# Kernel tuning notes

Measured on AMD Instinct MI355X. Metric: run time of the kernel, lower is better.

Reference implementation:

```python
import jax, jax.numpy as jnp
import numpy as np

IN_FEATURES = 512
OUT_FEATURES = 10
NEURONS_STRUCTURES = [64, 128, 256, 512]
REPETITIONS = 5
NUM_ACTIVATIONS = 4  # relu, tanh, sigmoid, gelu (exact erf, matching torch nn.GELU)
NUM_MODELS = NUM_ACTIVATIONS * REPETITIONS * len(NEURONS_STRUCTURES)  # 80
TOTAL_HIDDEN = sum(NEURONS_STRUCTURES) * REPETITIONS * NUM_ACTIVATIONS  # 19200
BATCH = 1024


def _build_neuron_model_id():
    # Mirrors ParallelMLPs.__init__ construction order:
    # for act -> for rep -> for structure: assign consecutive model ids
    ids = []
    m = 0
    for _act in range(NUM_ACTIVATIONS):
        for _rep in range(REPETITIONS):
            for n in NEURONS_STRUCTURES:
                ids += [m] * n
                m += 1
    return np.asarray(ids, dtype=np.int32)


def setup_inputs() -> dict:
    key = jax.random.key(0)
    k1, k2, k3, k4, k5 = jax.random.split(key, 5)
    x = jax.random.normal(k1, (BATCH, IN_FEATURES), dtype=jnp.float32)
    hidden_w = jax.random.normal(k2, (TOTAL_HIDDEN, IN_FEATURES), dtype=jnp.float32) * 0.05
    hidden_b = jax.random.normal(k3, (TOTAL_HIDDEN,), dtype=jnp.float32) * 0.05
    out_w = jax.random.normal(k4, (OUT_FEATURES, TOTAL_HIDDEN), dtype=jnp.float32) * 0.05
    out_b = jax.random.normal(k5, (NUM_MODELS, OUT_FEATURES), dtype=jnp.float32) * 0.05
    neuron_model_id = jnp.asarray(_build_neuron_model_id())
    return {"x": x, "hidden_w": hidden_w, "hidden_b": hidden_b,
            "out_w": out_w, "out_b": out_b, "neuron_model_id": neuron_model_id}


def reference(x, hidden_w, hidden_b, out_w, out_b, neuron_model_id):
    # Shared hidden linear: [B, H]
    h = x @ hidden_w.T + hidden_b
    # Per-block activations on equal contiguous chunks of the hidden dim
    split = TOTAL_HIDDEN // NUM_ACTIVATIONS
    acts = [jax.nn.relu, jnp.tanh, jax.nn.sigmoid,
            lambda t: jax.nn.gelu(t, approximate=False)]
    a = jnp.concatenate(
        [f(h[:, i * split:(i + 1) * split]) for i, f in enumerate(acts)], axis=1)
    # Ragged grouped out-projection: contrib[h, b, o] = a[b, h] * out_w[o, h]
    contrib = a.T[:, :, None] * out_w.T[:, None, :]  # [H, B, O]
    grouped = jax.ops.segment_sum(contrib, neuron_model_id,
                                  num_segments=NUM_MODELS)  # [M, B, O]
    return jnp.transpose(grouped, (1, 0, 2)) + out_b[None, :, :]  # [B, M, O]
```

## Files before the change

### kernel.cpp

```cpp
#include <hip/hip_runtime.h>
#include <hip/hip_bf16.h>
#include <cstdint>
#include <cstddef>


typedef unsigned short u16;
typedef unsigned int u32;
typedef __bf16 bf16x8 __attribute__((ext_vector_type(8)));
typedef float f32x4 __attribute__((ext_vector_type(4)));

__device__ __forceinline__ u16 f2bf(float f) {
  u32 u = __builtin_bit_cast(u32, f);
  u += 0x7fffu + ((u >> 16) & 1u);
  return (u16)(u >> 16);
}

__device__ __forceinline__ void async16(void* l, const void* g) {
  __builtin_amdgcn_global_load_lds(
      (__attribute__((address_space(1))) void*)(void*)g,
      (__attribute__((address_space(3))) void*)l, 16, 0, 0);
}

__global__ __launch_bounds__(256) void cvt_kernel(
    const float4* __restrict__ xs, uint2* __restrict__ xd, int nx4,
    const float4* __restrict__ ws, uint2* __restrict__ wd, int nw4) {
  int i = blockIdx.x * blockDim.x + threadIdx.x;
  if (i >= nx4 + nw4) return;
  const float4* s; uint2* d; int j;
  if (i < nx4) { s = xs; d = xd; j = i; }
  else         { s = ws; d = wd; j = i - nx4; }
  float4 f = s[j];
  uint2 o;
  o.x = (u32)f2bf(f.x) | ((u32)f2bf(f.y) << 16);
  o.y = (u32)f2bf(f.z) | ((u32)f2bf(f.w) << 16);
  d[j] = o;
}

__global__ __launch_bounds__(256, 2) void gemm_act_kernel(
    const u16* __restrict__ A,
    const u16* __restrict__ Bw,
    const float* __restrict__ hbias,
    u16* __restrict__ aout) {
  __shared__ char lds[65536];
  const int t = threadIdx.x;
  const int lane = t & 63;
  const int w = t >> 6;
  const int c = blockIdx.x & 7;
  const int L = c * 150 + (blockIdx.x >> 3);
  const int bx = L >> 3;
  const int by = L & 7;
  const int row0 = by * 128;
  const int col0 = bx * 128;
  const int wr = w >> 1, wc = w & 1;

  f32x4 acc[4][4];
#pragma unroll
  for (int m = 0; m < 4; ++m)
#pragma unroll
    for (int n = 0; n < 4; ++n)
#pragma unroll
      for (int r = 0; r < 4; ++r) acc[m][n][r] = 0.f;

  const int srow = t >> 3;
  const int sc8 = t & 7;

  auto stage = [&](int buf, int kt) {
    const int c8 = sc8 ^ (srow & 7);
    const int k0 = kt * 64 + c8 * 8;
#pragma unroll
    for (int i = 0; i < 4; ++i) {
      int row = i * 32 + srow;
      async16(lds + buf * 16384 + i * 4096 + w * 1024,
              A + (size_t)(row0 + row) * 512 + k0);
      async16(lds + 32768 + buf * 16384 + i * 4096 + w * 1024,
              Bw + (size_t)(col0 + row) * 512 + k0);
    }
  };

  const int il = lane & 15, q = lane >> 4;

  auto compute = [&](int buf) {
    const char* bA = lds + buf * 16384;
    const char* bB = lds + 32768 + buf * 16384;
#pragma unroll
    for (int ks = 0; ks < 2; ++ks) {
      bf16x8 av[4], bv[4];
#pragma unroll
      for (int m = 0; m < 4; ++m) {
        int row = wr * 64 + m * 16 + il;
        av[m] = *(const bf16x8*)(bA + row * 128 +
                                 ((ks * 64 + q * 16) ^ ((row & 7) << 4)));
      }
#pragma unroll
      for (int n = 0; n < 4; ++n) {
        int row = wc * 64 + n * 16 + il;
        bv[n] = *(const bf16x8*)(bB + row * 128 +
                                 ((ks * 64 + q * 16) ^ ((row & 7) << 4)));
      }
#pragma unroll
      for (int m = 0; m < 4; ++m)
#pragma unroll
        for (int n = 0; n < 4; ++n)
          acc[m][n] = __builtin_amdgcn_mfma_f32_16x16x32_bf16(av[m], bv[n],
                                                              acc[m][n], 0, 0, 0);
    }
  };

  stage(0, 0);
  stage(1, 1);
#pragma unroll
  for (int kt = 0; kt < 8; ++kt) {
    if (kt < 7) asm volatile("s_waitcnt vmcnt(8)" ::: "memory");
    else        asm volatile("s_waitcnt vmcnt(0)" ::: "memory");
    __builtin_amdgcn_s_barrier();
    compute(kt & 1);
    asm volatile("" ::: "memory");
    __builtin_amdgcn_s_barrier();
    if (kt < 6) stage(kt & 1, kt + 2);
  }

#pragma unroll
  for (int n = 0; n < 4; ++n) {
    int gcol = col0 + wc * 64 + n * 16 + il;
    int act = gcol / 4800;
    float bias = hbias[gcol];
#pragma unroll
    for (int m = 0; m < 4; ++m) {
      int growb = row0 + wr * 64 + m * 16 + q * 4;
#pragma unroll
      for (int r = 0; r < 4; ++r) {
        float v = acc[m][n][r] + bias;
        float o;
        if (act == 0)      o = fmaxf(v, 0.f);
        else if (act == 1) {
          float e = __expf(-2.f * fabsf(v));
          o = copysignf((1.f - e) / (1.f + e), v);
        }
        else if (act == 2) o = 1.f / (1.f + __expf(-v));
        else               o = 0.5f * v * (1.f + erff(v * 0.70710678118f));
        aout[(size_t)(growb + r) * 19200 + gcol] = f2bf(o);
      }
    }
  }
}

__global__ __launch_bounds__(256) void layer2_kernel(
    const u16* __restrict__ a,
    const float* __restrict__ ow,
    const float* __restrict__ ob,
    float* __restrict__ out) {
  const int t = threadIdx.x;
  const int lane = t & 63;
  const int w = t >> 6;
  const int m = blockIdx.x % 80;
  const int bt = blockIdx.x / 80;
  const int b0 = bt * 64 + w * 16;
  const int s = m & 3;
  const int rep = (m >> 2) % 5;
  const int act = m / 20;
  const int seg0 = act * 4800 + rep * 960 + 64 * ((1 << s) - 1);
  const int K = 64 << s;
  const int il = lane & 15, q = lane >> 4;

  f32x4 acc = {0.f, 0.f, 0.f, 0.f};
  const u16* arow = a + (size_t)(b0 + il) * 19200 + seg0 + q * 8;
  const float* wrow = ow + il * 19200 + seg0 + q * 8;
  const bool wvalid = il < 10;

  for (int k0 = 0; k0 < K; k0 += 32) {
    bf16x8 af = *(const bf16x8*)(arow + k0);
    union { bf16x8 v; u16 u[8]; } bb;
    if (wvalid) {
      float4 f0 = *(const float4*)(wrow + k0);
      float4 f1 = *(const float4*)(wrow + k0 + 4);
      bb.u[0] = f2bf(f0.x); bb.u[1] = f2bf(f0.y);
      bb.u[2] = f2bf(f0.z); bb.u[3] = f2bf(f0.w);
      bb.u[4] = f2bf(f1.x); bb.u[5] = f2bf(f1.y);
      bb.u[6] = f2bf(f1.z); bb.u[7] = f2bf(f1.w);
    } else {
#pragma unroll
      for (int j = 0; j < 8; ++j) bb.u[j] = 0;
    }
    acc = __builtin_amdgcn_mfma_f32_16x16x32_bf16(af, bb.v, acc, 0, 0, 0);
  }

  if (il < 10) {
    float bias = ob[m * 10 + il];
#pragma unroll
    for (int r = 0; r < 4; ++r)
      out[(size_t)(b0 + q * 4 + r) * 800 + m * 10 + il] = acc[r] + bias;
  }
}

extern "C" void kernel_launch(void* const* d_in, const int* in_sizes, int n_in,
                              void* d_out, int out_size, void* d_ws, size_t ws_size,
                              hipStream_t stream) {
  const float* x = (const float*)d_in[0];
  const float* hw = (const float*)d_in[1];
  const float* hb = (const float*)d_in[2];
  const float* ow = (const float*)d_in[3];
  const float* ob = (const float*)d_in[4];
  float* out = (float*)d_out;

  char* ws = (char*)d_ws;
  u16* xb = (u16*)ws;
  u16* wb = (u16*)(ws + 1048576);
  u16* ab = (u16*)(ws + 1048576 + 19660800);

  const int nx4 = (1024 * 512) / 4;
  const int nw4 = (19200 * 512) / 4;
  const int tot = nx4 + nw4;
  cvt_kernel<<<tot / 256, 256, 0, stream>>>((const float4*)x, (uint2*)xb, nx4,
                                            (const float4*)hw, (uint2*)wb, nw4);
  gemm_act_kernel<<<1200, 256, 0, stream>>>(xb, wb, hb, ab);
  layer2_kernel<<<1280, 256, 0, stream>>>(ab, ow, ob, out);
}
```

Before: 177.0 us.

## Halve GEMM K-tile to raise occupancy and unroll layer2 with dual accumulators

The hidden GEMM now stages K=32 slices instead of K=64, which halves LDS to 32 KB. The launch-bounds occupancy target rises from 2 to 5 blocks per CU, and the swizzle, staging loads and wait counts are adjusted to match. The goal is more resident waves to hide global-load latency, at the cost of twice as many barriers and smaller loads per stage. The layer-2 kernel processes 64 K per iteration with two independent MFMA accumulators to increase ILP.

```diff
diff --git a/kernel.cpp b/kernel.cpp
--- a/kernel.cpp
+++ b/kernel.cpp
@@ -36,12 +36,12 @@
   d[j] = o;
 }
 
-__global__ __launch_bounds__(256, 2) void gemm_act_kernel(
+__global__ __launch_bounds__(256, 5) void gemm_act_kernel(
     const u16* __restrict__ A,
     const u16* __restrict__ Bw,
     const float* __restrict__ hbias,
     u16* __restrict__ aout) {
-  __shared__ char lds[65536];
+  __shared__ char lds[32768];
   const int t = threadIdx.x;
   const int lane = t & 63;
   const int w = t >> 6;
@@ -61,18 +61,18 @@
 #pragma unroll
       for (int r = 0; r < 4; ++r) acc[m][n][r] = 0.f;
 
-  const int srow = t >> 3;
-  const int sc8 = t & 7;
+  const int srow = t >> 2;
+  const int sc4 = t & 3;
 
   auto stage = [&](int buf, int kt) {
-    const int c8 = sc8 ^ (srow & 7);
-    const int k0 = kt * 64 + c8 * 8;
-#pragma unroll
-    for (int i = 0; i < 4; ++i) {
-      int row = i * 32 + srow;
-      async16(lds + buf * 16384 + i * 4096 + w * 1024,
+    const int c4 = sc4 ^ ((srow >> 1) & 3);
+    const int k0 = kt * 32 + c4 * 8;
+#pragma unroll
+    for (int i = 0; i < 2; ++i) {
+      int row = i * 64 + srow;
+      async16(lds + buf * 8192 + i * 4096 + w * 1024,
               A + (size_t)(row0 + row) * 512 + k0);
-      async16(lds + 32768 + buf * 16384 + i * 4096 + w * 1024,
+      async16(lds + 16384 + buf * 8192 + i * 4096 + w * 1024,
               Bw + (size_t)(col0 + row) * 512 + k0);
     }
   };
@@ -80,43 +80,40 @@
   const int il = lane & 15, q = lane >> 4;
 
   auto compute = [&](int buf) {
-    const char* bA = lds + buf * 16384;
-    const char* bB = lds + 32768 + buf * 16384;
-#pragma unroll
-    for (int ks = 0; ks < 2; ++ks) {
-      bf16x8 av[4], bv[4];
-#pragma unroll
-      for (int m = 0; m < 4; ++m) {
-        int row = wr * 64 + m * 16 + il;
-        av[m] = *(const bf16x8*)(bA + row * 128 +
-                                 ((ks * 64 + q * 16) ^ ((row & 7) << 4)));
-      }
-#pragma unroll
-      for (int n = 0; n < 4; ++n) {
-        int row = wc * 64 + n * 16 + il;
-        bv[n] = *(const bf16x8*)(bB + row * 128 +
-                                 ((ks * 64 + q * 16) ^ ((row & 7) << 4)));
-      }
-#pragma unroll
-      for (int m = 0; m < 4; ++m)
-#pragma unroll
-        for (int n = 0; n < 4; ++n)
-          acc[m][n] = __builtin_amdgcn_mfma_f32_16x16x32_bf16(av[m], bv[n],
-                                                              acc[m][n], 0, 0, 0);
-    }
+    const char* bA = lds + buf * 8192;
+    const char* bB = lds + 16384 + buf * 8192;
+    bf16x8 av[4], bv[4];
+#pragma unroll
+    for (int m = 0; m < 4; ++m) {
+      int row = wr * 64 + m * 16 + il;
+      av[m] = *(const bf16x8*)(bA + row * 64 +
+                               ((q * 16) ^ (((row >> 1) & 3) << 4)));
+    }
+#pragma unroll
+    for (int n = 0; n < 4; ++n) {
+      int row = wc * 64 + n * 16 + il;
+      bv[n] = *(const bf16x8*)(bB + row * 64 +
+                               ((q * 16) ^ (((row >> 1) & 3) << 4)));
+    }
+#pragma unroll
+    for (int m = 0; m < 4; ++m)
+#pragma unroll
+      for (int n = 0; n < 4; ++n)
+        acc[m][n] = __builtin_amdgcn_mfma_f32_16x16x32_bf16(av[m], bv[n],
+                                                            acc[m][n], 0, 0, 0);
   };
 
   stage(0, 0);
   stage(1, 1);
-#pragma unroll
-  for (int kt = 0; kt < 8; ++kt) {
-    if (kt < 7) asm volatile("s_waitcnt vmcnt(8)" ::: "memory");
-    else        asm volatile("s_waitcnt vmcnt(0)" ::: "memory");
+#pragma unroll 4
+  for (int kt = 0; kt < 16; ++kt) {
+    if (kt < 15) asm volatile("s_waitcnt vmcnt(4)" ::: "memory");
+    else         asm volatile("s_waitcnt vmcnt(0)" ::: "memory");
     __builtin_amdgcn_s_barrier();
     compute(kt & 1);
     asm volatile("" ::: "memory");
     __builtin_amdgcn_s_barrier();
-    if (kt < 6) stage(kt & 1, kt + 2);
+    if (kt < 14) stage(kt & 1, kt + 2);
   }
 
 #pragma unroll
@@ -162,33 +159,42 @@
   const int K = 64 << s;
   const int il = lane & 15, q = lane >> 4;
 
-  f32x4 acc = {0.f, 0.f, 0.f, 0.f};
+  f32x4 acc0 = {0.f, 0.f, 0.f, 0.f};
+  f32x4 acc1 = {0.f, 0.f, 0.f, 0.f};
   const u16* arow = a + (size_t)(b0 + il) * 19200 + seg0 + q * 8;
   const float* wrow = ow + il * 19200 + seg0 + q * 8;
   const bool wvalid = il < 10;
 
-  for (int k0 = 0; k0 < K; k0 += 32) {
-    bf16x8 af = *(const bf16x8*)(arow + k0);
-    union { bf16x8 v; u16 u[8]; } bb;
+  for (int k0 = 0; k0 < K; k0 += 64) {
+    bf16x8 af0 = *(const bf16x8*)(arow + k0);
+    bf16x8 af1 = *(const bf16x8*)(arow + k0 + 32);
+    union { bf16x8 v; u16 u[8]; } b0u, b1u;
     if (wvalid) {
       float4 f0 = *(const float4*)(wrow + k0);
       float4 f1 = *(const float4*)(wrow + k0 + 4);
-      bb.u[0] = f2bf(f0.x); bb.u[1] = f2bf(f0.y);
-      bb.u[2] = f2bf(f0.z); bb.u[3] = f2bf(f0.w);
-      bb.u[4] = f2bf(f1.x); bb.u[5] = f2bf(f1.y);
-      bb.u[6] = f2bf(f1.z); bb.u[7] = f2bf(f1.w);
+      float4 f2 = *(const float4*)(wrow + k0 + 32);
+      float4 f3 = *(const float4*)(wrow + k0 + 36);
+      b0u.u[0] = f2bf(f0.x); b0u.u[1] = f2bf(f0.y);
+      b0u.u[2] = f2bf(f0.z); b0u.u[3] = f2bf(f0.w);
+      b0u.u[4] = f2bf(f1.x); b0u.u[5] = f2bf(f1.y);
+      b0u.u[6] = f2bf(f1.z); b0u.u[7] = f2bf(f1.w);
+      b1u.u[0] = f2bf(f2.x); b1u.u[1] = f2bf(f2.y);
+      b1u.u[2] = f2bf(f2.z); b1u.u[3] = f2bf(f2.w);
+      b1u.u[4] = f2bf(f3.x); b1u.u[5] = f2bf(f3.y);
+      b1u.u[6] = f2bf(f3.z); b1u.u[7] = f2bf(f3.w);
     } else {
 #pragma unroll
-      for (int j = 0; j < 8; ++j) bb.u[j] = 0;
-    }
-    acc = __builtin_amdgcn_mfma_f32_16x16x32_bf16(af, bb.v, acc, 0, 0, 0);
+      for (int j = 0; j < 8; ++j) { b0u.u[j] = 0; b1u.u[j] = 0; }
+    }
+    acc0 = __builtin_amdgcn_mfma_f32_16x16x32_bf16(af0, b0u.v, acc0, 0, 0, 0);
+    acc1 = __builtin_amdgcn_mfma_f32_16x16x32_bf16(af1, b1u.v, acc1, 0, 0, 0);
   }
 
   if (il < 10) {
     float bias = ob[m * 10 + il];
 #pragma unroll
     for (int r = 0; r < 4; ++r)
-      out[(size_t)(b0 + q * 4 + r) * 800 + m * 10 + il] = acc[r] + bias;
+      out[(size_t)(b0 + q * 4 + r) * 800 + m * 10 + il] = acc0[r] + acc1[r] + bias;
   }
 }
 
```

Result: slower. 222.9 us (+25.9%).
